# Performance work log

Measured on AMD Instinct MI355X. Metric: run time of the kernel, lower is better.

Reference implementation:

```python
import jax, jax.numpy as jnp
import numpy as np

N, E, F, H, O = 50000, 800000, 64, 128, 64
GRID_SIZE, SPLINE_ORDER = 3, 2


def make_grid(in_features, grid_size=GRID_SIZE, spline_order=SPLINE_ORDER, grid_range=(-1.0, 1.0)):
    h = (grid_range[1] - grid_range[0]) / grid_size
    pts = jnp.arange(-spline_order, grid_size + spline_order + 1, dtype=jnp.float32) * h + grid_range[0]
    return jnp.tile(pts[None, :], (in_features, 1))  # [in, grid_size + 2*order + 1]


def b_splines(x, grid, spline_order=SPLINE_ORDER):
    # x: [B, in], grid: [in, G+2k+1] -> bases [B, in, G+k]
    xe = x[..., None]
    bases = ((xe >= grid[:, :-1]) & (xe < grid[:, 1:])).astype(x.dtype)
    for k in range(1, spline_order + 1):
        bases = ((xe - grid[:, : -(k + 1)]) / (grid[:, k:-1] - grid[:, : -(k + 1)]) * bases[..., :-1]
                 + (grid[:, k + 1:] - xe) / (grid[:, k + 1:] - grid[:, 1:-k]) * bases[..., 1:])
    return bases


def setup_inputs() -> dict:
    key = jax.random.key(0)
    ks = jax.random.split(key, 12)
    x = jax.random.normal(ks[0], (N, F), dtype=jnp.float32)
    contexts = jax.random.normal(ks[1], (E, F), dtype=jnp.float32)
    attn = jax.random.uniform(ks[2], (E,), dtype=jnp.float32)
    seg_ids = jnp.sort(jax.random.randint(ks[3], (E,), 0, N, dtype=jnp.int32))
    s = 0.05
    Wn = jax.random.normal(ks[4], (H, F), dtype=jnp.float32) * s
    bn = jnp.zeros((H,), dtype=jnp.float32)
    Wc = jax.random.normal(ks[5], (H, F), dtype=jnp.float32) * s
    bc = jnp.zeros((H,), dtype=jnp.float32)
    Wu = jax.random.normal(ks[6], (O, H), dtype=jnp.float32) * s
    bu = jnp.zeros((O,), dtype=jnp.float32)
    n_coef = GRID_SIZE + SPLINE_ORDER
    base_w = jax.random.normal(ks[7], (O, O), dtype=jnp.float32) * s
    spline_w = jax.random.normal(ks[8], (O, O, n_coef), dtype=jnp.float32) * s
    spline_scaler = jnp.ones((O, O), dtype=jnp.float32)
    grid = make_grid(O)
    return dict(x=x, contexts=contexts, attn=attn, seg_ids=seg_ids, Wn=Wn, bn=bn,
                Wc=Wc, bc=bc, Wu=Wu, bu=bu, base_w=base_w, spline_w=spline_w,
                spline_scaler=spline_scaler, grid=grid)


def reference(x, contexts, attn, seg_ids, Wn, bn, Wc, bc, Wu, bu, base_w, spline_w, spline_scaler, grid):
    n = x.shape[0]
    # per-edge context transform, attention weighting
    ctx_t = contexts @ Wc.T + bc                      # [E, H]
    weighted = ctx_t * attn[:, None]                  # [E, H]
    seg_sum = jax.ops.segment_sum(weighted, seg_ids, num_segments=n)        # [N, H]
    deg = jax.ops.segment_sum(jnp.ones_like(attn), seg_ids, num_segments=n)  # [N]
    ctx_agg = seg_sum / jnp.maximum(deg, 1.0)[:, None]  # mean over edges per node
    x_t = x @ Wn.T + bn                               # [N, H]
    upd = (x_t + ctx_agg) @ Wu.T + bu                 # [N, O]
    # KANLinear (efficient-kan): silu base path + b-spline path
    base_out = jax.nn.silu(upd) @ base_w.T            # [N, O]
    bases = b_splines(upd, grid)                      # [N, O, G+k]
    scaled_sw = spline_w * spline_scaler[..., None]   # [O, O, G+k]
    spline_out = jnp.einsum('bik,oik->bo', bases, scaled_sw)
    kan_out = base_out + spline_out
    # nodes with no contexts keep their raw features (num_features == output_dim)
    return jnp.where(deg[:, None] > 0, kan_out, x)
```

## Files before the change

kernel.cpp:

```cpp
#include <hip/hip_runtime.h>
#include <hip/hip_bf16.h>

#define NN 50000
#define NE 800000

typedef short short8 __attribute__((ext_vector_type(8)));
typedef float f32x4 __attribute__((ext_vector_type(4)));
typedef unsigned short ushort_t;

static __device__ __forceinline__ unsigned bits(float f) { return __float_as_uint(f); }
static __device__ __forceinline__ float hi_f(float v) {
  return __uint_as_float(bits(v) & 0xFFFF0000u);
}
static __device__ __forceinline__ ushort_t hi_u(float v) { return (ushort_t)(bits(v) >> 16); }
static __device__ __forceinline__ unsigned pack_hi(float v0, float v1) {
  return (bits(v0) >> 16) | (bits(v1) & 0xFFFF0000u);
}
static __device__ __forceinline__ unsigned pack_lo(float v0, float v1) {
  float l0 = v0 - hi_f(v0), l1 = v1 - hi_f(v1);
  return (bits(l0) >> 16) | (bits(l1) & 0xFFFF0000u);
}

#define MFMA(a, b, c) __builtin_amdgcn_mfma_f32_16x16x32_bf16(a, b, c, 0, 0, 0)

__global__ __launch_bounds__(256) void kA_pack_off(
    const float* __restrict__ Wn, const float* __restrict__ Wc,
    const float* __restrict__ Wu, const float* __restrict__ base_w,
    const float* __restrict__ spline_w, const float* __restrict__ scaler,
    const int* __restrict__ seg,
    ushort_t* __restrict__ p1h, ushort_t* __restrict__ p2h,
    ushort_t* __restrict__ p3h, int* __restrict__ off) {
  int t = blockIdx.x * 256 + threadIdx.x;
  if (t < 4096) {
    int l = t & 63, lm = l & 15, lk = l >> 4;
    if (t < 2048) {
      int nt = t >> 8, ks = (t >> 6) & 3;
      int h = nt * 16 + lm;
#pragma unroll
      for (int j = 0; j < 8; ++j) {
        int f = ks * 32 + lk * 8 + j;
        float v = (f < 64) ? Wn[h * 64 + f] : Wc[h * 64 + (f - 64)];
        p1h[t * 8 + j] = hi_u(v);
      }
    }
    if (t < 1024) {
      int nt = t >> 8, ks = (t >> 6) & 3;
      int o = nt * 16 + lm;
#pragma unroll
      for (int j = 0; j < 8; ++j) {
        int hh = ks * 32 + lk * 8 + j;
        p2h[t * 8 + j] = hi_u(Wu[o * 128 + hh]);
      }
    }
    if (t < 3072) {
      int nt = t / 768, ks = (t >> 6) % 12;
      int o = nt * 16 + lm;
#pragma unroll
      for (int j = 0; j < 8; ++j) {
        int k = ks * 32 + lk * 8 + j;
        int i = k / 6, c = k % 6;
        float v = (c == 0) ? base_w[o * 64 + i]
                           : spline_w[(o * 64 + i) * 5 + (c - 1)] * scaler[o * 64 + i];
        p3h[t * 8 + j] = hi_u(v);
      }
    }
  }
  int e = t;
  if (e < NE) {
    int s1 = seg[e];
    if (e == 0) {
      for (int n = 0; n <= s1; ++n) off[n] = 0;
    } else {
      int s0 = seg[e - 1];
      for (int n = s0 + 1; n <= s1; ++n) off[n] = e;
    }
    if (e == NE - 1) {
      for (int n = s1 + 1; n <= NN; ++n) off[n] = NE;
    }
  }
}

__global__ __launch_bounds__(256) void k1_edge_agg(
    const float* __restrict__ contexts, const float* __restrict__ attn,
    const int* __restrict__ off, ushort_t* __restrict__ Sph,
    float* __restrict__ aprime, float* __restrict__ degw) {
  int n = blockIdx.x * 4 + (threadIdx.x >> 6);
  int lane = threadIdx.x & 63;
  if (n >= NN) return;
  int s = off[n];
  int e_end = off[n + 1];
  int deg_i = e_end - s;

  int sub = lane >> 4;
  int fq = lane & 15;
  const float4* ctx4 = (const float4*)contexts;

  float4 S = make_float4(0.f, 0.f, 0.f, 0.f);
  float A = 0.f;
  if (deg_i > 0) {
    int last = e_end - 1;
    for (int e0 = s; e0 < e_end; e0 += 16) {
      float a[4];
      float4 c[4];
#pragma unroll
      for (int u = 0; u < 4; ++u) {
        int eu = e0 + 4 * u + sub;
        a[u] = (eu < e_end) ? attn[eu] : 0.f;
        c[u] = ctx4[(size_t)min(eu, last) * 16 + fq];
      }
#pragma unroll
      for (int u = 0; u < 4; ++u) {
        S.x += a[u] * c[u].x;
        S.y += a[u] * c[u].y;
        S.z += a[u] * c[u].z;
        S.w += a[u] * c[u].w;
        A += a[u];
      }
    }
  }
#pragma unroll
  for (int m = 16; m <= 32; m <<= 1) {
    S.x += __shfl_xor(S.x, m);
    S.y += __shfl_xor(S.y, m);
    S.z += __shfl_xor(S.z, m);
    S.w += __shfl_xor(S.w, m);
    A += __shfl_xor(A, m);
  }
  float deg = (float)deg_i;
  float inv = 1.f / fmaxf(deg, 1.f);
  if (lane < 16) {
    float ox = S.x * inv, oy = S.y * inv, oz = S.z * inv, ow = S.w * inv;
    uint2 hp;
    hp.x = pack_hi(ox, oy);
    hp.y = pack_hi(oz, ow);
    *(uint2*)&Sph[(size_t)n * 64 + lane * 4] = hp;
  }
  if (lane == 0) { aprime[n] = A * inv; degw[n] = deg; }
}

__global__ __launch_bounds__(256, 6) void k234(
    const float* __restrict__ x,
    const ushort_t* __restrict__ Sph,
    const float* __restrict__ aprime, const float* __restrict__ degw,
    const float* __restrict__ bn, const float* __restrict__ bc,
    const float* __restrict__ bu,
    const ushort_t* __restrict__ p1h, const ushort_t* __restrict__ p2h,
    const ushort_t* __restrict__ p3h,
    const float* __restrict__ gridp, float* __restrict__ out) {
  __shared__ __align__(16) unsigned char arena[24576];
  __shared__ float ap[32], degl[32];
  ushort_t* Uh = (ushort_t*)arena;
  ushort_t* Ul = (ushort_t*)(arena + 8192);
  ushort_t* Th = (ushort_t*)(arena + 16384);
  ushort_t* Vh = (ushort_t*)arena;
  float*    ot = (float*)arena;

  int tid = threadIdx.x;
  int n0 = blockIdx.x * 32;
  int w = tid >> 6, l = tid & 63;
  int lm = l & 15, lk = l >> 4;
  const short8* P1h = (const short8*)p1h;
  const short8* P2h = (const short8*)p2h;
  const short8* P3h = (const short8*)p3h;
  int swzA = (lm & 7) << 3;

  {
    const float4* x4 = (const float4*)x;
    const uint4* Sh4 = (const uint4*)Sph;
#pragma unroll
    for (int q = tid; q < 512; q += 256) {
      int row = q >> 4, slot = q & 15;
      int n = n0 + row;
      int idx = (row * 128 + slot * 8) ^ ((row & 7) << 3);
      if (slot < 8) {
        float4 a = make_float4(0.f, 0.f, 0.f, 0.f), b = a;
        if (n < NN) {
          a = x4[(size_t)n * 16 + slot * 2];
          b = x4[(size_t)n * 16 + slot * 2 + 1];
        }
        uint4 hp, lp;
        hp.x = pack_hi(a.x, a.y); hp.y = pack_hi(a.z, a.w);
        hp.z = pack_hi(b.x, b.y); hp.w = pack_hi(b.z, b.w);
        lp.x = pack_lo(a.x, a.y); lp.y = pack_lo(a.z, a.w);
        lp.z = pack_lo(b.x, b.y); lp.w = pack_lo(b.z, b.w);
        *(uint4*)&Uh[idx] = hp;
        *(uint4*)&Ul[idx] = lp;
      } else {
        uint4 vh = make_uint4(0u, 0u, 0u, 0u);
        if (n < NN) vh = Sh4[(size_t)n * 8 + (slot & 7)];
        *(uint4*)&Uh[idx] = vh;
      }
    }
  }
  if (tid < 32) {
    int n = n0 + tid;
    ap[tid] = (n < NN) ? aprime[n] : 0.f;
    degl[tid] = (n < NN) ? degw[n] : 1.f;
  }
  __syncthreads();

  f32x4 acc1[2][2];
#pragma unroll
  for (int q = 0; q < 2; ++q)
#pragma unroll
    for (int mt = 0; mt < 2; ++mt) acc1[q][mt] = (f32x4){0.f, 0.f, 0.f, 0.f};
#pragma unroll
  for (int ks = 0; ks < 4; ++ks) {
    short8 bh0 = P1h[((2 * w + 0) * 4 + ks) * 64 + l];
    short8 bh1 = P1h[((2 * w + 1) * 4 + ks) * 64 + l];
#pragma unroll
    for (int mt = 0; mt < 2; ++mt) {
      int ai = ((mt * 16 + lm) * 128 + ks * 32 + lk * 8) ^ swzA;
      short8 ah = *(const short8*)&Uh[ai];
      acc1[0][mt] = MFMA(ah, bh0, acc1[0][mt]);
      acc1[1][mt] = MFMA(ah, bh1, acc1[1][mt]);
      if (ks < 2) {
        short8 al = *(const short8*)&Ul[ai];
        acc1[0][mt] = MFMA(al, bh0, acc1[0][mt]);
        acc1[1][mt] = MFMA(al, bh1, acc1[1][mt]);
      }
    }
  }
#pragma unroll
  for (int q = 0; q < 2; ++q) {
    int h = (2 * w + q) * 16 + lm;
    float bnv = bn[h], bcv = bc[h];
#pragma unroll
    for (int mt = 0; mt < 2; ++mt) {
#pragma unroll
      for (int r = 0; r < 4; ++r) {
        int node = mt * 16 + lk * 4 + r;
        float t = acc1[q][mt][r] + bnv + ap[node] * bcv;
        Th[(node * 128 + h) ^ ((node & 7) << 3)] = hi_u(t);
      }
    }
  }
  __syncthreads();

  f32x4 acc2[2];
  acc2[0] = (f32x4){0.f, 0.f, 0.f, 0.f};
  acc2[1] = (f32x4){0.f, 0.f, 0.f, 0.f};
#pragma unroll
  for (int ks = 0; ks < 4; ++ks) {
    short8 bh = P2h[(w * 4 + ks) * 64 + l];
#pragma unroll
    for (int mt = 0; mt < 2; ++mt) {
      int ai = ((mt * 16 + lm) * 128 + ks * 32 + lk * 8) ^ swzA;
      short8 ah = *(const short8*)&Th[ai];
      acc2[mt] = MFMA(ah, bh, acc2[mt]);
    }
  }
  __syncthreads();

  float g[8];
#pragma unroll
  for (int j = 0; j < 8; ++j) g[j] = gridp[j];
  float r1[7], r2[6];
#pragma unroll
  for (int j = 0; j < 7; ++j) r1[j] = 1.f / (g[j + 1] - g[j]);
#pragma unroll
  for (int j = 0; j < 6; ++j) r2[j] = 1.f / (g[j + 2] - g[j]);
  float buv = bu[w * 16 + lm];

#pragma unroll
  for (int mt = 0; mt < 2; ++mt) {
#pragma unroll
    for (int r = 0; r < 4; ++r) {
      float xv = acc2[mt][r] + buv;
      float sil = xv / (1.f + __expf(-xv));
      float b0[7], b1[6], b2[5];
#pragma unroll
      for (int q = 0; q < 7; ++q) b0[q] = (xv >= g[q] && xv < g[q + 1]) ? 1.f : 0.f;
#pragma unroll
      for (int q = 0; q < 6; ++q)
        b1[q] = (xv - g[q]) * r1[q] * b0[q] + (g[q + 2] - xv) * r1[q + 1] * b0[q + 1];
#pragma unroll
      for (int q = 0; q < 5; ++q)
        b2[q] = (xv - g[q]) * r2[q] * b1[q] + (g[q + 3] - xv) * r2[q + 1] * b1[q + 1];
      int ln = mt * 16 + lk * 4 + r;
      int base = ln * 384 + (w * 16 + lm) * 6;
      int sw = (ln & 7) << 3;
      *(unsigned*)&Vh[(base + 0) ^ sw] = pack_hi(sil, b2[0]);
      *(unsigned*)&Vh[(base + 2) ^ sw] = pack_hi(b2[1], b2[2]);
      *(unsigned*)&Vh[(base + 4) ^ sw] = pack_hi(b2[3], b2[4]);
    }
  }
  __syncthreads();

  f32x4 accK[2];
  accK[0] = (f32x4){0.f, 0.f, 0.f, 0.f};
  accK[1] = (f32x4){0.f, 0.f, 0.f, 0.f};
#pragma unroll
  for (int ks = 0; ks < 12; ++ks) {
    short8 bh = P3h[(w * 12 + ks) * 64 + l];
#pragma unroll
    for (int s = 0; s < 2; ++s) {
      int ri = ((s * 16 + lm) * 384 + ks * 32 + lk * 8) ^ swzA;
      short8 ah = *(const short8*)&Vh[ri];
      accK[s] = MFMA(ah, bh, accK[s]);
    }
  }
  __syncthreads();

#pragma unroll
  for (int s = 0; s < 2; ++s) {
    int o = w * 16 + lm;
#pragma unroll
    for (int r = 0; r < 4; ++r) {
      int ln = s * 16 + lk * 4 + r;
      ot[(ln * 64 + o) ^ ((ln & 7) << 3)] = accK[s][r];
    }
  }
  __syncthreads();

  {
    int row2 = tid >> 3, c8 = (tid & 7) * 8;
    int n = n0 + row2;
    if (n < NN) {
      int sw = (row2 & 7) << 3;
      float4 v0 = *(float4*)&ot[((row2 * 64 + c8) ^ sw)];
      float4 v1 = *(float4*)&ot[((row2 * 64 + c8 + 4) ^ sw)];
      if (degl[row2] <= 0.f) {
        v0 = *(const float4*)(x + (size_t)n * 64 + c8);
        v1 = *(const float4*)(x + (size_t)n * 64 + c8 + 4);
      }
      *(float4*)(out + (size_t)n * 64 + c8) = v0;
      *(float4*)(out + (size_t)n * 64 + c8 + 4) = v1;
    }
  }
}

extern "C" void kernel_launch(void* const* d_in, const int* in_sizes, int n_in,
                              void* d_out, int out_size, void* d_ws, size_t ws_size,
                              hipStream_t stream) {
  const float* x        = (const float*)d_in[0];
  const float* contexts = (const float*)d_in[1];
  const float* attn     = (const float*)d_in[2];
  const int*   seg      = (const int*)d_in[3];
  const float* Wn       = (const float*)d_in[4];
  const float* bn       = (const float*)d_in[5];
  const float* Wc       = (const float*)d_in[6];
  const float* bc       = (const float*)d_in[7];
  const float* Wu       = (const float*)d_in[8];
  const float* bu       = (const float*)d_in[9];
  const float* base_w   = (const float*)d_in[10];
  const float* spline_w = (const float*)d_in[11];
  const float* scaler   = (const float*)d_in[12];
  const float* gridp    = (const float*)d_in[13];
  float* out = (float*)d_out;

  ushort_t* us  = (ushort_t*)d_ws;
  ushort_t* Sph = us;
  ushort_t* p1h = Sph + 3200000;
  ushort_t* p2h = p1h + 16384;
  ushort_t* p3h = p2h + 8192;
  float* aprime = (float*)(p3h + 24576);
  float* degw   = aprime + 50000;
  int*   off    = (int*)(degw + 50000);

  kA_pack_off<<<3125, 256, 0, stream>>>(Wn, Wc, Wu, base_w, spline_w, scaler, seg,
                                        p1h, p2h, p3h, off);
  k1_edge_agg<<<12500, 256, 0, stream>>>(contexts, attn, off, Sph, aprime, degw);
  k234<<<1563, 256, 0, stream>>>(x, Sph, aprime, degw, bn, bc, bu,
                                 p1h, p2h, p3h, gridp, out);
}
```

Baseline: 67.54 us.

## Merge edge aggregation and node MLP into one kernel with interleaved halves

Replaces the separate edge-aggregation and node-transform kernels with one dual-role kernel. The first launch aggregates the first half of the nodes. The second launch interleaves aggregation blocks for the second half with MLP/KAN blocks for the first half, so memory-bound gather work overlaps MFMA compute. The third launch finishes the MLP for the second half. It relies on stream ordering between launches for correctness. It adds occupancy limits from the shared launch bounds and LDS allocation to the aggregation blocks.

```diff
diff --git a/kernel.cpp b/kernel.cpp
--- a/kernel.cpp
+++ b/kernel.cpp
@@ -3,6 +3,7 @@
 
 #define NN 50000
 #define NE 800000
+#define HALF_N 25024
 
 typedef short short8 __attribute__((ext_vector_type(8)));
 typedef float f32x4 __attribute__((ext_vector_type(4)));
@@ -80,68 +81,12 @@
   }
 }
 
-__global__ __launch_bounds__(256) void k1_edge_agg(
+__global__ __launch_bounds__(256, 6) void kMix(
+    int eBase, int eEnd, int gBase, int gTiles, int stride,
+    const float* __restrict__ x,
     const float* __restrict__ contexts, const float* __restrict__ attn,
-    const int* __restrict__ off, ushort_t* __restrict__ Sph,
-    float* __restrict__ aprime, float* __restrict__ degw) {
-  int n = blockIdx.x * 4 + (threadIdx.x >> 6);
-  int lane = threadIdx.x & 63;
-  if (n >= NN) return;
-  int s = off[n];
-  int e_end = off[n + 1];
-  int deg_i = e_end - s;
-
-  int sub = lane >> 4;
-  int fq = lane & 15;
-  const float4* ctx4 = (const float4*)contexts;
-
-  float4 S = make_float4(0.f, 0.f, 0.f, 0.f);
-  float A = 0.f;
-  if (deg_i > 0) {
-    int last = e_end - 1;
-    for (int e0 = s; e0 < e_end; e0 += 16) {
-      float a[4];
-      float4 c[4];
-#pragma unroll
-      for (int u = 0; u < 4; ++u) {
-        int eu = e0 + 4 * u + sub;
-        a[u] = (eu < e_end) ? attn[eu] : 0.f;
-        c[u] = ctx4[(size_t)min(eu, last) * 16 + fq];
-      }
-#pragma unroll
-      for (int u = 0; u < 4; ++u) {
-        S.x += a[u] * c[u].x;
-        S.y += a[u] * c[u].y;
-        S.z += a[u] * c[u].z;
-        S.w += a[u] * c[u].w;
-        A += a[u];
-      }
-    }
-  }
-#pragma unroll
-  for (int m = 16; m <= 32; m <<= 1) {
-    S.x += __shfl_xor(S.x, m);
-    S.y += __shfl_xor(S.y, m);
-    S.z += __shfl_xor(S.z, m);
-    S.w += __shfl_xor(S.w, m);
-    A += __shfl_xor(A, m);
-  }
-  float deg = (float)deg_i;
-  float inv = 1.f / fmaxf(deg, 1.f);
-  if (lane < 16) {
-    float ox = S.x * inv, oy = S.y * inv, oz = S.z * inv, ow = S.w * inv;
-    uint2 hp;
-    hp.x = pack_hi(ox, oy);
-    hp.y = pack_hi(oz, ow);
-    *(uint2*)&Sph[(size_t)n * 64 + lane * 4] = hp;
-  }
-  if (lane == 0) { aprime[n] = A * inv; degw[n] = deg; }
-}
-
-__global__ __launch_bounds__(256, 6) void k234(
-    const float* __restrict__ x,
-    const ushort_t* __restrict__ Sph,
-    const float* __restrict__ aprime, const float* __restrict__ degw,
+    const int* __restrict__ off,
+    ushort_t* __restrict__ Sph, float* __restrict__ aprime, float* __restrict__ degw,
     const float* __restrict__ bn, const float* __restrict__ bc,
     const float* __restrict__ bu,
     const ushort_t* __restrict__ p1h, const ushort_t* __restrict__ p2h,
@@ -149,14 +94,83 @@
     const float* __restrict__ gridp, float* __restrict__ out) {
   __shared__ __align__(16) unsigned char arena[24576];
   __shared__ float ap[32], degl[32];
+
+  int b = blockIdx.x;
+  int tid = threadIdx.x;
+  bool isG;
+  int g = 0, eIdx = 0;
+  if (stride == 0) { isG = false; eIdx = b; }
+  else if (stride == 1) { isG = true; g = b; }
+  else {
+    int q = b / stride, r = b - q * stride;
+    if (r == stride - 1) { isG = true; g = q; }
+    else { isG = false; eIdx = q * (stride - 1) + r; }
+  }
+
+  if (!isG) {
+    int n = eBase + eIdx * 4 + (tid >> 6);
+    int lane = tid & 63;
+    if (n >= eEnd) return;
+    int s = off[n];
+    int e_end = off[n + 1];
+    int deg_i = e_end - s;
+
+    int sub = lane >> 4;
+    int fq = lane & 15;
+    const float4* ctx4 = (const float4*)contexts;
+
+    float4 S = make_float4(0.f, 0.f, 0.f, 0.f);
+    float A = 0.f;
+    if (deg_i > 0) {
+      int last = e_end - 1;
+      for (int e0 = s; e0 < e_end; e0 += 16) {
+        float a[4];
+        float4 c[4];
+#pragma unroll
+        for (int u = 0; u < 4; ++u) {
+          int eu = e0 + 4 * u + sub;
+          a[u] = (eu < e_end) ? attn[eu] : 0.f;
+          c[u] = ctx4[(size_t)min(eu, last) * 16 + fq];
+        }
+#pragma unroll
+        for (int u = 0; u < 4; ++u) {
+          S.x += a[u] * c[u].x;
+          S.y += a[u] * c[u].y;
+          S.z += a[u] * c[u].z;
+          S.w += a[u] * c[u].w;
+          A += a[u];
+        }
+      }
+    }
+#pragma unroll
+    for (int m = 16; m <= 32; m <<= 1) {
+      S.x += __shfl_xor(S.x, m);
+      S.y += __shfl_xor(S.y, m);
+      S.z += __shfl_xor(S.z, m);
+      S.w += __shfl_xor(S.w, m);
+      A += __shfl_xor(A, m);
+    }
+    float deg = (float)deg_i;
+    float inv = 1.f / fmaxf(deg, 1.f);
+    if (lane < 16) {
+      float ox = S.x * inv, oy = S.y * inv, oz = S.z * inv, ow = S.w * inv;
+      uint2 hp;
+      hp.x = pack_hi(ox, oy);
+      hp.y = pack_hi(oz, ow);
+      *(uint2*)&Sph[(size_t)n * 64 + lane * 4] = hp;
+    }
+    if (lane == 0) { aprime[n] = A * inv; degw[n] = deg; }
+    return;
+  }
+
+  if (g >= gTiles) return;
   ushort_t* Uh = (ushort_t*)arena;
   ushort_t* Ul = (ushort_t*)(arena + 8192);
   ushort_t* Th = (ushort_t*)(arena + 16384);
   ushort_t* Vh = (ushort_t*)arena;
   float*    ot = (float*)arena;
 
-  int tid = threadIdx.x;
-  int n0 = blockIdx.x * 32;
+  int n0 = gBase + g * 32;
   int w = tid >> 6, l = tid & 63;
   int lm = l & 15, lk = l >> 4;
   const short8* P1h = (const short8*)p1h;
@@ -173,16 +187,16 @@
       int n = n0 + row;
       int idx = (row * 128 + slot * 8) ^ ((row & 7) << 3);
       if (slot < 8) {
-        float4 a = make_float4(0.f, 0.f, 0.f, 0.f), b = a;
+        float4 a = make_float4(0.f, 0.f, 0.f, 0.f), bb = a;
         if (n < NN) {
           a = x4[(size_t)n * 16 + slot * 2];
-          b = x4[(size_t)n * 16 + slot * 2 + 1];
+          bb = x4[(size_t)n * 16 + slot * 2 + 1];
         }
         uint4 hp, lp;
         hp.x = pack_hi(a.x, a.y); hp.y = pack_hi(a.z, a.w);
-        hp.z = pack_hi(b.x, b.y); hp.w = pack_hi(b.z, b.w);
+        hp.z = pack_hi(bb.x, bb.y); hp.w = pack_hi(bb.z, bb.w);
         lp.x = pack_lo(a.x, a.y); lp.y = pack_lo(a.z, a.w);
-        lp.z = pack_lo(b.x, b.y); lp.w = pack_lo(b.z, b.w);
+        lp.z = pack_lo(bb.x, bb.y); lp.w = pack_lo(bb.z, bb.w);
         *(uint4*)&Uh[idx] = hp;
         *(uint4*)&Ul[idx] = lp;
       } else {
@@ -252,14 +266,14 @@
   }
   __syncthreads();
 
-  float g[8];
-#pragma unroll
-  for (int j = 0; j < 8; ++j) g[j] = gridp[j];
+  float g8[8];
+#pragma unroll
+  for (int j = 0; j < 8; ++j) g8[j] = gridp[j];
   float r1[7], r2[6];
 #pragma unroll
-  for (int j = 0; j < 7; ++j) r1[j] = 1.f / (g[j + 1] - g[j]);
-#pragma unroll
-  for (int j = 0; j < 6; ++j) r2[j] = 1.f / (g[j + 2] - g[j]);
+  for (int j = 0; j < 7; ++j) r1[j] = 1.f / (g8[j + 1] - g8[j]);
+#pragma unroll
+  for (int j = 0; j < 6; ++j) r2[j] = 1.f / (g8[j + 2] - g8[j]);
   float buv = bu[w * 16 + lm];
 
 #pragma unroll
@@ -270,13 +284,13 @@
       float sil = xv / (1.f + __expf(-xv));
       float b0[7], b1[6], b2[5];
 #pragma unroll
-      for (int q = 0; q < 7; ++q) b0[q] = (xv >= g[q] && xv < g[q + 1]) ? 1.f : 0.f;
+      for (int q = 0; q < 7; ++q) b0[q] = (xv >= g8[q] && xv < g8[q + 1]) ? 1.f : 0.f;
 #pragma unroll
       for (int q = 0; q < 6; ++q)
-        b1[q] = (xv - g[q]) * r1[q] * b0[q] + (g[q + 2] - xv) * r1[q + 1] * b0[q + 1];
+        b1[q] = (xv - g8[q]) * r1[q] * b0[q] + (g8[q + 2] - xv) * r1[q + 1] * b0[q + 1];
 #pragma unroll
       for (int q = 0; q < 5; ++q)
-        b2[q] = (xv - g[q]) * r2[q] * b1[q] + (g[q + 3] - xv) * r2[q + 1] * b1[q + 1];
+        b2[q] = (xv - g8[q]) * r2[q] * b1[q] + (g8[q + 3] - xv) * r2[q + 1] * b1[q + 1];
       int ln = mt * 16 + lk * 4 + r;
       int base = ln * 384 + (w * 16 + lm) * 6;
       int sw = (ln & 7) << 3;
@@ -360,7 +374,13 @@
 
   kA_pack_off<<<3125, 256, 0, stream>>>(Wn, Wc, Wu, base_w, spline_w, scaler, seg,
                                         p1h, p2h, p3h, off);
-  k1_edge_agg<<<12500, 256, 0, stream>>>(contexts, attn, off, Sph, aprime, degw);
-  k234<<<1563, 256, 0, stream>>>(x, Sph, aprime, degw, bn, bc, bu,
-                                 p1h, p2h, p3h, gridp, out);
-}
+  kMix<<<6256, 256, 0, stream>>>(0, HALF_N, 0, 0, 0,
+                                 x, contexts, attn, off, Sph, aprime, degw,
+                                 bn, bc, bu, p1h, p2h, p3h, gridp, out);
+  kMix<<<7038, 256, 0, stream>>>(HALF_N, NN, 0, 782, 9,
+                                 x, contexts, attn, off, Sph, aprime, degw,
+                                 bn, bc, bu, p1h, p2h, p3h, gridp, out);
+  kMix<<<781, 256, 0, stream>>>(0, 0, HALF_N, 781, 1,
+                                x, contexts, attn, off, Sph, aprime, degw,
+                                bn, bc, bu, p1h, p2h, p3h, gridp, out);
+}
```

Result: slower. 71.24 us (+5.5%).

## Fold Wu into Wn/Wc to merge two node GEMMs into one

Applied to the files above, without the earlier changes.

Precomputes the fused weight Wu·[Wn|Wc] and the bias terms Wu·bn and Wu·bc in the pack kernel. The node kernel then runs a single 128→64 MFMA GEMM straight to the update vector, with no intermediate hidden tile, its shared-memory round trip or the extra barrier. This removes roughly half the MFMA work in the node stage. It changes rounding because the fused weight is truncated to bf16 after the product rather than before, and the pack kernel now does a small serial dot product per thread.

```diff
diff --git a/kernel.cpp b/kernel.cpp
--- a/kernel.cpp
+++ b/kernel.cpp
@@ -25,45 +25,54 @@
 
 __global__ __launch_bounds__(256) void kA_pack_off(
     const float* __restrict__ Wn, const float* __restrict__ Wc,
-    const float* __restrict__ Wu, const float* __restrict__ base_w,
-    const float* __restrict__ spline_w, const float* __restrict__ scaler,
-    const int* __restrict__ seg,
-    ushort_t* __restrict__ p1h, ushort_t* __restrict__ p2h,
-    ushort_t* __restrict__ p3h, int* __restrict__ off) {
+    const float* __restrict__ Wu, const float* __restrict__ bn,
+    const float* __restrict__ bc,
+    const float* __restrict__ base_w, const float* __restrict__ spline_w,
+    const float* __restrict__ scaler, const int* __restrict__ seg,
+    ushort_t* __restrict__ p2f, ushort_t* __restrict__ p3h,
+    float* __restrict__ c12, int* __restrict__ off) {
   int t = blockIdx.x * 256 + threadIdx.x;
-  if (t < 4096) {
-    int l = t & 63, lm = l & 15, lk = l >> 4;
-    if (t < 2048) {
-      int nt = t >> 8, ks = (t >> 6) & 3;
-      int h = nt * 16 + lm;
-#pragma unroll
-      for (int j = 0; j < 8; ++j) {
-        int f = ks * 32 + lk * 8 + j;
-        float v = (f < 64) ? Wn[h * 64 + f] : Wc[h * 64 + (f - 64)];
-        p1h[t * 8 + j] = hi_u(v);
-      }
-    }
-    if (t < 1024) {
-      int nt = t >> 8, ks = (t >> 6) & 3;
-      int o = nt * 16 + lm;
-#pragma unroll
-      for (int j = 0; j < 8; ++j) {
-        int hh = ks * 32 + lk * 8 + j;
-        p2h[t * 8 + j] = hi_u(Wu[o * 128 + hh]);
-      }
-    }
-    if (t < 3072) {
-      int nt = t / 768, ks = (t >> 6) % 12;
-      int o = nt * 16 + lm;
-#pragma unroll
-      for (int j = 0; j < 8; ++j) {
-        int k = ks * 32 + lk * 8 + j;
-        int i = k / 6, c = k % 6;
-        float v = (c == 0) ? base_w[o * 64 + i]
-                           : spline_w[(o * 64 + i) * 5 + (c - 1)] * scaler[o * 64 + i];
-        p3h[t * 8 + j] = hi_u(v);
-      }
-    }
+  if (t < 8192) {
+    int o = t >> 7, f = t & 127;
+    float acc = 0.f;
+    const float* wu = Wu + o * 128;
+    if (f < 64) {
+#pragma unroll 4
+      for (int h = 0; h < 128; ++h) acc += wu[h] * Wn[h * 64 + f];
+    } else {
+      int f2 = f - 64;
+#pragma unroll 4
+      for (int h = 0; h < 128; ++h) acc += wu[h] * Wc[h * 64 + f2];
+    }
+    int nt = o >> 4, lm = o & 15;
+    int ks = f >> 5, rem = f & 31, lk = rem >> 3, j = rem & 7;
+    p2f[(((nt * 4 + ks) * 64) + lk * 16 + lm) * 8 + j] = hi_u(acc);
+  }
+  int t2 = t - 8192;
+  if (t2 >= 0 && t2 < 3072) {
+    int l = t2 & 63, lm = l & 15, lk = l >> 4;
+    int nt = t2 / 768, ks = (t2 >> 6) % 12;
+    int o = nt * 16 + lm;
+#pragma unroll
+    for (int j = 0; j < 8; ++j) {
+      int k = ks * 32 + lk * 8 + j;
+      int i = k / 6, c = k % 6;
+      float v = (c == 0) ? base_w[o * 64 + i]
+                         : spline_w[(o * 64 + i) * 5 + (c - 1)] * scaler[o * 64 + i];
+      p3h[t2 * 8 + j] = hi_u(v);
+    }
+  }
+  int t3 = t - 11264;
+  if (t3 >= 0 && t3 < 64) {
+    float a1 = 0.f, a2 = 0.f;
+    const float* wu = Wu + t3 * 128;
+#pragma unroll 4
+    for (int h = 0; h < 128; ++h) {
+      a1 += wu[h] * bn[h];
+      a2 += wu[h] * bc[h];
+    }
+    c12[t3] = a1;
+    c12[64 + t3] = a2;
   }
   int e = t;
   if (e < NE) {
@@ -138,20 +147,17 @@
   if (lane == 0) { aprime[n] = A * inv; degw[n] = deg; }
 }
 
-__global__ __launch_bounds__(256, 6) void k234(
+__global__ __launch_bounds__(256, 6) void k24(
     const float* __restrict__ x,
     const ushort_t* __restrict__ Sph,
     const float* __restrict__ aprime, const float* __restrict__ degw,
-    const float* __restrict__ bn, const float* __restrict__ bc,
-    const float* __restrict__ bu,
-    const ushort_t* __restrict__ p1h, const ushort_t* __restrict__ p2h,
-    const ushort_t* __restrict__ p3h,
+    const float* __restrict__ bu, const float* __restrict__ c12,
+    const ushort_t* __restrict__ p2f, const ushort_t* __restrict__ p3h,
     const float* __restrict__ gridp, float* __restrict__ out) {
   __shared__ __align__(16) unsigned char arena[24576];
   __shared__ float ap[32], degl[32];
   ushort_t* Uh = (ushort_t*)arena;
   ushort_t* Ul = (ushort_t*)(arena + 8192);
-  ushort_t* Th = (ushort_t*)(arena + 16384);
   ushort_t* Vh = (ushort_t*)arena;
   float*    ot = (float*)arena;
 
@@ -159,8 +165,7 @@
   int n0 = blockIdx.x * 32;
   int w = tid >> 6, l = tid & 63;
   int lm = l & 15, lk = l >> 4;
-  const short8* P1h = (const short8*)p1h;
-  const short8* P2h = (const short8*)p2h;
+  const short8* P2f = (const short8*)p2f;
   const short8* P3h = (const short8*)p3h;
   int swzA = (lm & 7) << 3;
 
@@ -199,87 +204,55 @@
   }
   __syncthreads();
 
-  f32x4 acc1[2][2];
-#pragma unroll
-  for (int q = 0; q < 2; ++q)
-#pragma unroll
-    for (int mt = 0; mt < 2; ++mt) acc1[q][mt] = (f32x4){0.f, 0.f, 0.f, 0.f};
+  f32x4 acc2[2];
+  acc2[0] = (f32x4){0.f, 0.f, 0.f, 0.f};
+  acc2[1] = (f32x4){0.f, 0.f, 0.f, 0.f};
 #pragma unroll
   for (int ks = 0; ks < 4; ++ks) {
-    short8 bh0 = P1h[((2 * w + 0) * 4 + ks) * 64 + l];
-    short8 bh1 = P1h[((2 * w + 1) * 4 + ks) * 64 + l];
+    short8 bh = P2f[(w * 4 + ks) * 64 + l];
 #pragma unroll
     for (int mt = 0; mt < 2; ++mt) {
       int ai = ((mt * 16 + lm) * 128 + ks * 32 + lk * 8) ^ swzA;
       short8 ah = *(const short8*)&Uh[ai];
-      acc1[0][mt] = MFMA(ah, bh0, acc1[0][mt]);
-      acc1[1][mt] = MFMA(ah, bh1, acc1[1][mt]);
+      acc2[mt] = MFMA(ah, bh, acc2[mt]);
       if (ks < 2) {
         short8 al = *(const short8*)&Ul[ai];
-        acc1[0][mt] = MFMA(al, bh0, acc1[0][mt]);
-        acc1[1][mt] = MFMA(al, bh1, acc1[1][mt]);
-      }
-    }
-  }
-#pragma unroll
-  for (int q = 0; q < 2; ++q) {
-    int h = (2 * w + q) * 16 + lm;
-    float bnv = bn[h], bcv = bc[h];
-#pragma unroll
-    for (int mt = 0; mt < 2; ++mt) {
-#pragma unroll
-      for (int r = 0; r < 4; ++r) {
-        int node = mt * 16 + lk * 4 + r;
-        float t = acc1[q][mt][r] + bnv + ap[node] * bcv;
-        Th[(node * 128 + h) ^ ((node & 7) << 3)] = hi_u(t);
-      }
-    }
-  }
-  __syncthreads();
-
-  f32x4 acc2[2];
-  acc2[0] = (f32x4){0.f, 0.f, 0.f, 0.f};
-  acc2[1] = (f32x4){0.f, 0.f, 0.f, 0.f};
-#pragma unroll
-  for (int ks = 0; ks < 4; ++ks) {
-    short8 bh = P2h[(w * 4 + ks) * 64 + l];
-#pragma unroll
-    for (int mt = 0; mt < 2; ++mt) {
-      int ai = ((mt * 16 + lm) * 128 + ks * 32 + lk * 8) ^ swzA;
-      short8 ah = *(const short8*)&Th[ai];
-      acc2[mt] = MFMA(ah, bh, acc2[mt]);
-    }
-  }
-  __syncthreads();
-
-  float g[8];
-#pragma unroll
-  for (int j = 0; j < 8; ++j) g[j] = gridp[j];
+        acc2[mt] = MFMA(al, bh, acc2[mt]);
+      }
+    }
+  }
+  __syncthreads();
+
+  int o = w * 16 + lm;
+  float cb = c12[o] + bu[o];
+  float c2v = c12[64 + o];
+  float g8[8];
+#pragma unroll
+  for (int j = 0; j < 8; ++j) g8[j] = gridp[j];
   float r1[7], r2[6];
 #pragma unroll
-  for (int j = 0; j < 7; ++j) r1[j] = 1.f / (g[j + 1] - g[j]);
-#pragma unroll
-  for (int j = 0; j < 6; ++j) r2[j] = 1.f / (g[j + 2] - g[j]);
-  float buv = bu[w * 16 + lm];
+  for (int j = 0; j < 7; ++j) r1[j] = 1.f / (g8[j + 1] - g8[j]);
+#pragma unroll
+  for (int j = 0; j < 6; ++j) r2[j] = 1.f / (g8[j + 2] - g8[j]);
 
 #pragma unroll
   for (int mt = 0; mt < 2; ++mt) {
 #pragma unroll
     for (int r = 0; r < 4; ++r) {
-      float xv = acc2[mt][r] + buv;
+      int node = mt * 16 + lk * 4 + r;
+      float xv = acc2[mt][r] + cb + ap[node] * c2v;
       float sil = xv / (1.f + __expf(-xv));
       float b0[7], b1[6], b2[5];
 #pragma unroll
-      for (int q = 0; q < 7; ++q) b0[q] = (xv >= g[q] && xv < g[q + 1]) ? 1.f : 0.f;
+      for (int q = 0; q < 7; ++q) b0[q] = (xv >= g8[q] && xv < g8[q + 1]) ? 1.f : 0.f;
 #pragma unroll
       for (int q = 0; q < 6; ++q)
-        b1[q] = (xv - g[q]) * r1[q] * b0[q] + (g[q + 2] - xv) * r1[q + 1] * b0[q + 1];
+        b1[q] = (xv - g8[q]) * r1[q] * b0[q] + (g8[q + 2] - xv) * r1[q + 1] * b0[q + 1];
 #pragma unroll
       for (int q = 0; q < 5; ++q)
-        b2[q] = (xv - g[q]) * r2[q] * b1[q] + (g[q + 3] - xv) * r2[q + 1] * b1[q + 1];
-      int ln = mt * 16 + lk * 4 + r;
-      int base = ln * 384 + (w * 16 + lm) * 6;
-      int sw = (ln & 7) << 3;
+        b2[q] = (xv - g8[q]) * r2[q] * b1[q] + (g8[q + 3] - xv) * r2[q + 1] * b1[q + 1];
+      int base = node * 384 + o * 6;
+      int sw = (node & 7) << 3;
       *(unsigned*)&Vh[(base + 0) ^ sw] = pack_hi(sil, b2[0]);
       *(unsigned*)&Vh[(base + 2) ^ sw] = pack_hi(b2[1], b2[2]);
       *(unsigned*)&Vh[(base + 4) ^ sw] = pack_hi(b2[3], b2[4]);
@@ -304,7 +277,6 @@
 
 #pragma unroll
   for (int s = 0; s < 2; ++s) {
-    int o = w * 16 + lm;
 #pragma unroll
     for (int r = 0; r < 4; ++r) {
       int ln = s * 16 + lk * 4 + r;
@@ -351,16 +323,15 @@
 
   ushort_t* us  = (ushort_t*)d_ws;
   ushort_t* Sph = us;
-  ushort_t* p1h = Sph + 3200000;
-  ushort_t* p2h = p1h + 16384;
-  ushort_t* p3h = p2h + 8192;
-  float* aprime = (float*)(p3h + 24576);
+  ushort_t* p2f = Sph + 3200000;
+  ushort_t* p3h = p2f + 8192;
+  float* c12    = (float*)(p3h + 24576);
+  float* aprime = c12 + 128;
   float* degw   = aprime + 50000;
   int*   off    = (int*)(degw + 50000);
 
-  kA_pack_off<<<3125, 256, 0, stream>>>(Wn, Wc, Wu, base_w, spline_w, scaler, seg,
-                                        p1h, p2h, p3h, off);
+  kA_pack_off<<<3125, 256, 0, stream>>>(Wn, Wc, Wu, bn, bc, base_w, spline_w, scaler,
+                                        seg, p2f, p3h, c12, off);
   k1_edge_agg<<<12500, 256, 0, stream>>>(contexts, attn, off, Sph, aprime, degw);
-  k234<<<1563, 256, 0, stream>>>(x, Sph, aprime, degw, bn, bc, bu,
-                                 p1h, p2h, p3h, gridp, out);
-}
+  k24<<<1563, 256, 0, stream>>>(x, Sph, aprime, degw, bu, c12, p2f, p3h, gridp, out);
+}
```

Result: no change. 68.44 us (+1.3%).
